# Kernel optimization log

Hardware: AMD Instinct MI355X
Metric: run time of the kernel (lower is better)

## Reference

```python
import jax, jax.numpy as jnp
import numpy as np
import math

NEG_INF = -1e9  # keras Softmax masking uses a large negative additive constant

def setup_inputs() -> dict:
    key = jax.random.key(0)
    k1, k2, k3, k4 = jax.random.split(key, 4)
    B, T, C, H = 4, 4096, 1024, 128
    x = jax.random.normal(k1, (B, T, C), dtype=jnp.float32)
    Wq = jax.random.normal(k2, (C, H), dtype=jnp.float32) * (1.0 / math.sqrt(C))
    Wk = jax.random.normal(k3, (C, H), dtype=jnp.float32) * (1.0 / math.sqrt(C))
    Wv = jax.random.normal(k4, (C, H), dtype=jnp.float32) * (1.0 / math.sqrt(C))
    return {"x": x, "Wq": Wq, "Wk": Wk, "Wv": Wv}

def reference(x, Wq, Wk, Wv):
    # x: [B, T, C]; projections are bias-free Dense layers
    B, T, C = x.shape
    q = jnp.einsum('btc,ch->bth', x, Wq)  # [B, T, H]
    k = jnp.einsum('btc,ch->bth', x, Wk)  # [B, T, H]
    v = jnp.einsum('btc,ch->bth', x, Wv)  # [B, T, H]
    # NOTE: original scales by sqrt(C) (the input channel dim), not sqrt(head_size)
    wei = jnp.einsum('bth,bsh->bts', q, k) / math.sqrt(C)  # [B, T, T]
    causal = jnp.tril(jnp.ones((T, T), dtype=bool))
    wei = jnp.where(causal[None, :, :], wei, NEG_INF)
    wei = jax.nn.softmax(wei, axis=-1)
    # dropout is identity at inference
    out = jnp.einsum('bts,bsh->bth', wei, v)  # [B, T, H]
    return out
```

## Files before the change

kernel.cpp:

```cpp
#include <hip/hip_runtime.h>
#include <hip/hip_bf16.h>

typedef __bf16 bf16x8 __attribute__((ext_vector_type(8)));
typedef __bf16 bf16x4 __attribute__((ext_vector_type(4)));
typedef float  f32x4  __attribute__((ext_vector_type(4)));

#define NB 4
#define TT 4096
#define CC 1024
#define HH 128
#define PS 72
#define MNEG -30000.0f
#define NHV 31

__device__ inline void gload16(const void* g, void* l) {
  __builtin_amdgcn_global_load_lds(
      (const __attribute__((address_space(1))) void*)g,
      (__attribute__((address_space(3))) void*)l, 16, 0, 0);
}

__device__ __forceinline__ int probe_isbf(const unsigned int* __restrict__ xw) {
  int lane = threadIdx.x & 63;
  int cnt = 0;
#pragma unroll
  for (int i = 0; i < 4; ++i) {
    unsigned int w = xw[lane + 64 * i];
    int e = (int)((w >> 7) & 0xFFu);
    cnt += (e >= 100 && e <= 135) ? 1 : 0;
  }
  cnt += __shfl_xor(cnt, 1);  cnt += __shfl_xor(cnt, 2);  cnt += __shfl_xor(cnt, 4);
  cnt += __shfl_xor(cnt, 8);  cnt += __shfl_xor(cnt, 16); cnt += __shfl_xor(cnt, 32);
  return cnt >= 128;
}

__global__ __launch_bounds__(256) void transpose_w3(
    const void* __restrict__ Wq, const void* __restrict__ Wk,
    const void* __restrict__ Wv, __bf16* __restrict__ Wt,
    const unsigned int* __restrict__ xw) {
  int isbf = probe_isbf(xw);
  int which = blockIdx.y;
  const void* W = (which == 0) ? Wq : (which == 1) ? Wk : Wv;
  int idx = blockIdx.x * 256 + threadIdx.x;
  int h = idx & 127, c = idx >> 7;
  __bf16 val;
  if (isbf) val = ((const __bf16*)W)[c * HH + h];
  else      val = (__bf16)(((const float*)W)[c * HH + h]);
  size_t o = (size_t)(c >> 6) * 24576 + (size_t)which * 8192 +
             (size_t)((c >> 3) & 7) * 1024 + (size_t)h * 8 + (c & 7);
  Wt[o] = val;
}

__global__ __launch_bounds__(768) void qkv_proj(
    const void* __restrict__ x, const __bf16* __restrict__ Wt,
    __bf16* __restrict__ q, __bf16* __restrict__ ktl, __bf16* __restrict__ vtl) {
  __shared__ __align__(16) __bf16 XT[2][4096];
  __shared__ __align__(16) __bf16 WTs[2][24576];
  int isbf = probe_isbf((const unsigned int*)x);
  int tid = threadIdx.x, lane = tid & 63, wave = tid >> 6;
  int which = wave >> 2, rowgrp = wave & 3;
  int l16 = lane & 15, quad = lane >> 4;
  int row0 = blockIdx.x * 64;
  f32x4 acc[8] = {};

#define STAGE(ss, b)                                                          \
  for (int i = wave; i < 56; i += 12) {                                       \
    if (i < 8) {                                                              \
      int row = i * 8 + (lane >> 3), g = lane & 7;                            \
      bf16x8 pk;                                                              \
      if (isbf) {                                                             \
        pk = *(const bf16x8*)((const __bf16*)x + (size_t)(row0 + row) * CC +  \
                              (ss) * 64 + g * 8);                             \
      } else {                                                                \
        const float* xf = (const float*)x + (size_t)(row0 + row) * CC +       \
                          (ss) * 64 + g * 8;                                  \
        f32x4 lo = *(const f32x4*)xf;                                         \
        f32x4 hi = *(const f32x4*)(xf + 4);                                   \
        for (int j = 0; j < 4; ++j) { pk[j] = (__bf16)lo[j]; pk[j+4] = (__bf16)hi[j]; } \
      }                                                                       \
      *(bf16x8*)(&XT[b][g * 512 + (row ^ g) * 8]) = pk;                       \
    } else {                                                                  \
      int j = i - 8;                                                          \
      gload16(Wt + (size_t)(ss) * 24576 + j * 512 + lane * 8,                 \
              &WTs[b][j * 512]);                                              \
    }                                                                         \
  }

  STAGE(0, 0);
  for (int s = 0; s < 16; ++s) {
    int cb = s & 1;
    __syncthreads();
    if (s + 1 < 16) { STAGE(s + 1, cb ^ 1); }
#pragma unroll
    for (int t = 0; t < 2; ++t) {
      int g = t * 4 + quad;
      bf16x8 a = *(const bf16x8*)(&XT[cb][g * 512 + ((rowgrp * 16 + l16) ^ g) * 8]);
#pragma unroll
      for (int nt = 0; nt < 8; ++nt) {
        bf16x8 b = *(const bf16x8*)(&WTs[cb][(size_t)which * 8192 + g * 1024 + (nt * 16 + l16) * 8]);
        acc[nt] = __builtin_amdgcn_mfma_f32_16x16x32_bf16(a, b, acc[nt], 0, 0, 0);
      }
    }
  }
#undef STAGE

  int tile = row0 >> 6;
  if (which == 0) {
#pragma unroll
    for (int nt = 0; nt < 8; ++nt)
#pragma unroll
      for (int r = 0; r < 4; ++r) {
        int row = row0 + rowgrp * 16 + quad * 4 + r;
        q[(size_t)row * HH + nt * 16 + l16] = (__bf16)acc[nt][r];
      }
  } else if (which == 1) {
    __bf16* kb = ktl + (size_t)tile * 8192;
#pragma unroll
    for (int nt = 0; nt < 8; ++nt) {
      int h = nt * 16 + l16, g = h >> 3, j = h & 7;
#pragma unroll
      for (int r = 0; r < 4; ++r) {
        int sidx = rowgrp * 16 + quad * 4 + r;
        kb[g * 512 + sidx * 8 + j] = (__bf16)acc[nt][r];
      }
    }
  } else {
    __bf16* vb = vtl + (size_t)tile * 8192;
#pragma unroll
    for (int nt = 0; nt < 8; ++nt) {
      int h = nt * 16 + l16;
      int sb = rowgrp * 16 + quad * 4;
      bf16x4 pk;
#pragma unroll
      for (int r = 0; r < 4; ++r) pk[r] = (__bf16)acc[nt][r];
      *(bf16x4*)(vb + (sb >> 3) * 1024 + h * 8 + (sb & 7)) = pk;
    }
  }
}

__global__ __launch_bounds__(768, 3) void flash_attn_bal(
    const __bf16* __restrict__ q, const __bf16* __restrict__ ktl,
    const __bf16* __restrict__ vtl, void* __restrict__ out,
    const unsigned int* __restrict__ xw,
    float* __restrict__ partO, float* __restrict__ partL) {
  __shared__ __align__(16) __bf16 PL[12][16 * PS];
  __shared__ float CMB[2][64][132];
  __shared__ float CL[2][64];

  int bx = blockIdx.x;
  int batch = (bx & 7) >> 1;
  int qt0 = ((bx >> 3) << 1) | (bx & 1);

  int tid = threadIdx.x, lane = tid & 63, wave = tid >> 6;
  int kg = wave >> 2, rowgrp = wave & 3;
  int l16 = lane & 15, quad = lane >> 4;

  int isbf = probe_isbf(xw);
  const __bf16* qp  = q   + (size_t)batch * TT * HH;
  const __bf16* ktb = ktl + (size_t)batch * TT * HH;
  const __bf16* vtb = vtl + (size_t)batch * TT * HH;

  bf16x8 onesf;
#pragma unroll
  for (int j = 0; j < 8; ++j) onesf[j] = (l16 == 0) ? (__bf16)1.0f : (__bf16)0.0f;
  const float SC = 0.0450842200278f;
  const float M0 = 4.0f;

  for (int part = 0; part < 2; ++part) {
    int qtu, j0, j1;
    if (part == 0) { qtu = qt0; j0 = 0; j1 = min(qt0 + 1, 33); }
    else {
      if (qt0 > 30) break;
      qtu = 63 - qt0; j0 = 33; j1 = 64 - qt0;
    }
    int qb = qtu * 64;
    int qrl = qb + rowgrp * 16 + quad * 4;

    bf16x8 qf[4];
    {
      const __bf16* qrow = qp + (size_t)(qb + rowgrp * 16 + l16) * HH + quad * 8;
#pragma unroll
      for (int ks = 0; ks < 4; ++ks) qf[ks] = *(const bf16x8*)(qrow + ks * 32);
    }

    f32x4 acc[8] = {};
    f32x4 acc_l = {};

    for (int jt = j0 + kg; jt < j1; jt += 3) {
      const __bf16* kt  = ktb + (size_t)jt * 8192;
      const __bf16* vt2 = vtb + (size_t)jt * 8192;

      bf16x8 kf[4][4];
#pragma unroll
      for (int ks = 0; ks < 4; ++ks)
#pragma unroll
        for (int kn = 0; kn < 4; ++kn)
          kf[ks][kn] = *(const bf16x8*)(kt + ((4 * ks + quad) * 64 + kn * 16 + l16) * 8);

      f32x4 accs[4] = {};
#pragma unroll
      for (int ks = 0; ks < 4; ++ks)
#pragma unroll
        for (int kn = 0; kn < 4; ++kn)
          accs[kn] = __builtin_amdgcn_mfma_f32_16x16x32_bf16(qf[ks], kf[ks][kn], accs[kn], 0, 0, 0);

      bf16x8 vf[2][8];
#pragma unroll
      for (int ks2 = 0; ks2 < 2; ++ks2)
#pragma unroll
        for (int nt = 0; nt < 8; ++nt)
          vf[ks2][nt] = *(const bf16x8*)(vt2 + (ks2 * 4 + quad) * 1024 + (nt * 16 + l16) * 8);

      float pv[4][4];
      if (jt == qtu) {
#pragma unroll
        for (int nt = 0; nt < 4; ++nt) {
          int kcol = jt * 64 + nt * 16 + l16;
#pragma unroll
          for (int r = 0; r < 4; ++r) {
            float z = fmaf(accs[nt][r], SC, -M0);
            z = (kcol <= qrl + r) ? z : MNEG;
            pv[nt][r] = exp2f(z);
          }
        }
      } else {
#pragma unroll
        for (int nt = 0; nt < 4; ++nt)
#pragma unroll
          for (int r = 0; r < 4; ++r)
            pv[nt][r] = exp2f(fmaf(accs[nt][r], SC, -M0));
      }

      __bf16* pw = &PL[wave][0];
#pragma unroll
      for (int nt = 0; nt < 4; ++nt)
#pragma unroll
        for (int r = 0; r < 4; ++r)
          pw[(quad * 4 + r) * PS + nt * 16 + l16] = (__bf16)pv[nt][r];

#pragma unroll
      for (int ks2 = 0; ks2 < 2; ++ks2) {
        bf16x8 pa = *(const bf16x8*)(pw + l16 * PS + ks2 * 32 + quad * 8);
        acc_l = __builtin_amdgcn_mfma_f32_16x16x32_bf16(pa, onesf, acc_l, 0, 0, 0);
#pragma unroll
        for (int nt = 0; nt < 8; ++nt)
          acc[nt] = __builtin_amdgcn_mfma_f32_16x16x32_bf16(pa, vf[ks2][nt], acc[nt], 0, 0, 0);
      }
    }

    int rr = rowgrp * 16 + quad * 4;
    __syncthreads();
    if (kg > 0) {
#pragma unroll
      for (int nt = 0; nt < 8; ++nt)
#pragma unroll
        for (int r = 0; r < 4; ++r)
          CMB[kg - 1][rr + r][nt * 16 + l16] = acc[nt][r];
      if (l16 == 0) {
#pragma unroll
        for (int r = 0; r < 4; ++r) CL[kg - 1][rr + r] = acc_l[r];
      }
    }
    __syncthreads();
    if (kg == 0) {
      float lsum[4];
#pragma unroll
      for (int r = 0; r < 4; ++r) {
        float lr = __shfl(acc_l[r], lane & 48);
        lsum[r] = lr + CL[0][rr + r] + CL[1][rr + r];
      }
      if (part == 0 && qt0 <= 32) {
        __bf16* ob = (__bf16*)out + (size_t)batch * TT * HH;
        float*  of = (float*)out  + (size_t)batch * TT * HH;
        float inv[4];
#pragma unroll
        for (int r = 0; r < 4; ++r) inv[r] = 1.f / fmaxf(lsum[r], 1e-30f);
#pragma unroll
        for (int nt = 0; nt < 8; ++nt)
#pragma unroll
          for (int r = 0; r < 4; ++r) {
            int col = nt * 16 + l16;
            float val = (acc[nt][r] + CMB[0][rr + r][col] + CMB[1][rr + r][col]) * inv[r];
            size_t idx = (size_t)(qb + rr + r) * HH + col;
            if (isbf) ob[idx] = (__bf16)val;
            else      of[idx] = val;
          }
      } else {
        int slot = (batch * NHV + (qtu - 33)) * 2 + part;
        float* po = partO + (size_t)slot * 8192;
#pragma unroll
        for (int nt = 0; nt < 8; ++nt)
#pragma unroll
          for (int r = 0; r < 4; ++r) {
            int col = nt * 16 + l16;
            po[(rr + r) * 128 + col] = acc[nt][r] + CMB[0][rr + r][col] + CMB[1][rr + r][col];
          }
        if (l16 == 0) {
#pragma unroll
          for (int r = 0; r < 4; ++r) partL[slot * 64 + rr + r] = lsum[r];
        }
      }
    }
  }
}

__global__ __launch_bounds__(256) void combine2(
    const float* __restrict__ partO, const float* __restrict__ partL,
    void* __restrict__ out, const unsigned int* __restrict__ xw) {
  int bx = blockIdx.x;
  int batch = bx / NHV, qidx = bx % NHV;
  int Q = 33 + qidx;
  int slot0 = (batch * NHV + qidx) * 2;
  __shared__ float inv[64];
  int tid = threadIdx.x;
  if (tid < 64) {
    float L = partL[slot0 * 64 + tid] + partL[(slot0 + 1) * 64 + tid];
    inv[tid] = 1.f / fmaxf(L, 1e-30f);
  }
  __syncthreads();
  int isbf = probe_isbf(xw);
  size_t obase = (size_t)batch * TT * HH + (size_t)Q * 8192;
  const f32x4* p4 = (const f32x4*)partO;
#pragma unroll
  for (int i = 0; i < 8; ++i) {
    int e4 = i * 256 + tid;
    int row = e4 >> 5;
    f32x4 a = p4[(size_t)slot0 * 2048 + e4];
    f32x4 b = p4[(size_t)(slot0 + 1) * 2048 + e4];
    float w = inv[row];
    f32x4 v;
    v[0] = (a[0] + b[0]) * w; v[1] = (a[1] + b[1]) * w;
    v[2] = (a[2] + b[2]) * w; v[3] = (a[3] + b[3]) * w;
    if (isbf) {
      bf16x4 ob;
#pragma unroll
      for (int j = 0; j < 4; ++j) ob[j] = (__bf16)v[j];
      *(bf16x4*)((__bf16*)out + obase + (size_t)e4 * 4) = ob;
    } else {
      *(f32x4*)((float*)out + obase + (size_t)e4 * 4) = v;
    }
  }
}

__global__ __launch_bounds__(768, 3) void flash_attn_fb(
    const __bf16* __restrict__ q, const __bf16* __restrict__ ktl,
    const __bf16* __restrict__ vtl, void* __restrict__ out,
    const unsigned int* __restrict__ xw) {
  __shared__ __align__(16) __bf16 PLs[6][2][32 * PS];
  __shared__ float CMB[4][32][132];
  __shared__ float CL[4][32];

  int bx = blockIdx.x;
  int batch = (bx & 7) >> 1;
  int qt0 = ((bx >> 3) << 1) | (bx & 1);

  int tid = threadIdx.x, lane = tid & 63, wave = tid >> 6;
  int p = wave >> 1, rw = wave & 1;
  int l16 = lane & 15, quad = lane >> 4;

  int kA = (6 * (qt0 + 1) + 32) / 65;
  kA = max(1, min(5, kA));
  int qtB = 63 - qt0;
  int unit, kg, nkg, qtu, rbase;
  if (p < kA) { unit = 0; kg = p;      nkg = kA;     qtu = qt0; rbase = 0;  }
  else        { unit = 1; kg = p - kA; nkg = 6 - kA; qtu = qtB; rbase = 32; }

  int qb = qtu * 64;
  int MAXT = max(qt0 / kA + 1, qtB / (6 - kA) + 1);
  int mytrips = (qtu - kg) / nkg + 1;
  int isbf = probe_isbf(xw);

  const __bf16* qp  = q   + (size_t)batch * TT * HH;
  const __bf16* ktb = ktl + (size_t)batch * TT * HH;
  const __bf16* vtb = vtl + (size_t)batch * TT * HH;

  bf16x8 qf[2][4];
#pragma unroll
  for (int rg = 0; rg < 2; ++rg) {
    const __bf16* qrow = qp + (size_t)(qb + rbase + rg * 16 + l16) * HH + quad * 8;
#pragma unroll
    for (int ks = 0; ks < 4; ++ks) qf[rg][ks] = *(const bf16x8*)(qrow + ks * 32);
  }
  bf16x8 onesf;
#pragma unroll
  for (int j = 0; j < 8; ++j) onesf[j] = (l16 == 0) ? (__bf16)1.0f : (__bf16)0.0f;

  f32x4 acc_o[2][4] = {};
  f32x4 acc_l[2] = {};
  const float SC = 0.0450842200278f;
  const float M0 = 4.0f;

  for (int t = 0; t < MAXT; ++t) {
    int jt = kg + t * nkg;
    int valid = (t < mytrips);
    int jtc = valid ? jt : kg;
    const __bf16* kt  = ktb + (size_t)jtc * 8192;
    const __bf16* vt2 = vtb + (size_t)jtc * 8192;

    bf16x8 kf[4][2];
#pragma unroll
    for (int ks = 0; ks < 4; ++ks)
#pragma unroll
      for (int kn = 0; kn < 2; ++kn)
        kf[ks][kn] = *(const bf16x8*)(kt + ((4 * ks + quad) * 64 + (rw * 2 + kn) * 16 + l16) * 8);

    f32x4 accs[2][2] = {};
#pragma unroll
    for (int ks = 0; ks < 4; ++ks)
#pragma unroll
      for (int rg = 0; rg < 2; ++rg)
#pragma unroll
        for (int kn = 0; kn < 2; ++kn)
          accs[rg][kn] = __builtin_amdgcn_mfma_f32_16x16x32_bf16(qf[rg][ks], kf[ks][kn], accs[rg][kn], 0, 0, 0);

    bf16x8 vf[2][4];
#pragma unroll
    for (int ks2 = 0; ks2 < 2; ++ks2)
#pragma unroll
      for (int nt = 0; nt < 4; ++nt)
        vf[ks2][nt] = *(const bf16x8*)(vt2 + (ks2 * 4 + quad) * 1024 + (rw * 64 + nt * 16 + l16) * 8);

    float pv[2][2][4];
    if (valid && jt == qtu) {
#pragma unroll
      for (int rg = 0; rg < 2; ++rg)
#pragma unroll
        for (int kn = 0; kn < 2; ++kn) {
          int kcol = jt * 64 + (rw * 2 + kn) * 16 + l16;
          int qr0 = qb + rbase + rg * 16 + quad * 4;
#pragma unroll
          for (int r = 0; r < 4; ++r) {
            float z = fmaf(accs[rg][kn][r], SC, -M0);
            z = (kcol <= qr0 + r) ? z : MNEG;
            pv[rg][kn][r] = exp2f(z);
          }
        }
    } else if (valid) {
#pragma unroll
      for (int rg = 0; rg < 2; ++rg)
#pragma unroll
        for (int kn = 0; kn < 2; ++kn)
#pragma unroll
          for (int r = 0; r < 4; ++r)
            pv[rg][kn][r] = exp2f(fmaf(accs[rg][kn][r], SC, -M0));
    } else {
#pragma unroll
      for (int rg = 0; rg < 2; ++rg)
#pragma unroll
        for (int kn = 0; kn < 2; ++kn)
#pragma unroll
          for (int r = 0; r < 4; ++r)
            pv[rg][kn][r] = 0.0f;
    }

    __bf16* pw = &PLs[p][t & 1][0];
#pragma unroll
    for (int rg = 0; rg < 2; ++rg)
#pragma unroll
      for (int kn = 0; kn < 2; ++kn)
#pragma unroll
        for (int r = 0; r < 4; ++r)
          pw[(rg * 16 + quad * 4 + r) * PS + (rw * 2 + kn) * 16 + l16] = (__bf16)pv[rg][kn][r];

    __syncthreads();

#pragma unroll
    for (int ks2 = 0; ks2 < 2; ++ks2) {
      bf16x8 pa0 = *(const bf16x8*)(pw + l16 * PS + ks2 * 32 + quad * 8);
      bf16x8 pa1 = *(const bf16x8*)(pw + (16 + l16) * PS + ks2 * 32 + quad * 8);
      acc_l[0] = __builtin_amdgcn_mfma_f32_16x16x32_bf16(pa0, onesf, acc_l[0], 0, 0, 0);
      acc_l[1] = __builtin_amdgcn_mfma_f32_16x16x32_bf16(pa1, onesf, acc_l[1], 0, 0, 0);
#pragma unroll
      for (int nt = 0; nt < 4; ++nt) {
        acc_o[0][nt] = __builtin_amdgcn_mfma_f32_16x16x32_bf16(pa0, vf[ks2][nt], acc_o[0][nt], 0, 0, 0);
        acc_o[1][nt] = __builtin_amdgcn_mfma_f32_16x16x32_bf16(pa1, vf[ks2][nt], acc_o[1][nt], 0, 0, 0);
      }
    }
  }

  if (kg > 0) {
    int slot = (unit == 0) ? (kg - 1) : (kA - 1 + kg - 1);
#pragma unroll
    for (int rh = 0; rh < 2; ++rh)
#pragma unroll
      for (int nt = 0; nt < 4; ++nt)
#pragma unroll
        for (int r = 0; r < 4; ++r)
          CMB[slot][rh * 16 + quad * 4 + r][rw * 64 + nt * 16 + l16] = acc_o[rh][nt][r];
    if (rw == 0 && l16 == 0) {
#pragma unroll
      for (int rh = 0; rh < 2; ++rh)
#pragma unroll
        for (int r = 0; r < 4; ++r) CL[slot][rh * 16 + quad * 4 + r] = acc_l[rh][r];
    }
  }
  __syncthreads();
  if (kg == 0) {
    int lo  = (unit == 0) ? 0 : kA - 1;
    int cnt = (unit == 0) ? kA - 1 : 5 - kA;
    __bf16* ob = (__bf16*)out + (size_t)batch * TT * HH;
    float*  of = (float*)out  + (size_t)batch * TT * HH;
#pragma unroll
    for (int rh = 0; rh < 2; ++rh) {
      float inv[4];
#pragma unroll
      for (int r = 0; r < 4; ++r) {
        float lr = __shfl(acc_l[rh][r], lane & 48);
        for (int c = 0; c < cnt; ++c) lr += CL[lo + c][rh * 16 + quad * 4 + r];
        inv[r] = 1.f / fmaxf(lr, 1e-30f);
      }
#pragma unroll
      for (int nt = 0; nt < 4; ++nt)
#pragma unroll
        for (int r = 0; r < 4; ++r) {
          int row = qb + rbase + rh * 16 + quad * 4 + r;
          int col = rw * 64 + nt * 16 + l16;
          float val = acc_o[rh][nt][r];
          for (int c = 0; c < cnt; ++c) val += CMB[lo + c][rh * 16 + quad * 4 + r][col];
          val *= inv[r];
          size_t idx = (size_t)row * HH + col;
          if (isbf) ob[idx] = (__bf16)val;
          else      of[idx] = val;
        }
    }
  }
}

extern "C" void kernel_launch(void* const* d_in, const int* in_sizes, int n_in,
                              void* d_out, int out_size, void* d_ws, size_t ws_size,
                              hipStream_t stream) {
  const void* x  = d_in[0];
  const void* Wq = d_in[1];
  const void* Wk = d_in[2];
  const void* Wv = d_in[3];
  char* wsb = (char*)d_ws;
  __bf16* q   = (__bf16*)wsb;
  __bf16* ktl = q   + (size_t)NB * TT * HH;
  __bf16* vtl = ktl + (size_t)NB * TT * HH;
  __bf16* wt  = vtl + (size_t)NB * TT * HH;
  size_t base = (((size_t)(3 * NB * TT * HH + 3 * CC * HH) * 2) + 255) & ~(size_t)255;
  size_t needO = (size_t)NB * NHV * 2 * 8192 * 4;
  size_t needL = (size_t)NB * NHV * 2 * 64 * 4;
  float* partO = (float*)(wsb + base);
  float* partL = (float*)(wsb + base + needO);
  bool bal = (base + needO + needL) <= ws_size;
  (void)in_sizes; (void)n_in; (void)out_size;

  transpose_w3<<<dim3(512, 3), 256, 0, stream>>>(Wq, Wk, Wv, wt,
                                                 (const unsigned int*)x);
  qkv_proj<<<256, 768, 0, stream>>>(x, wt, q, ktl, vtl);
  if (bal) {
    flash_attn_bal<<<NB * 64, 768, 0, stream>>>(q, ktl, vtl, d_out,
                                                (const unsigned int*)x,
                                                partO, partL);
    combine2<<<NB * NHV, 256, 0, stream>>>(partO, partL, d_out,
                                           (const unsigned int*)x);
  } else {
    flash_attn_fb<<<NB * 64, 768, 0, stream>>>(q, ktl, vtl, d_out,
                                               (const unsigned int*)x);
  }
}
```

Measured before the change: 173.9 us.

## Fuse split-KV combine into attention kernel via inter-block flag handoff

Removes the separate combine2 kernel launch. Now only the part-1 block writes its partial O and L to the workspace and raises a per-tile flag. The part-0 block spins on that flag and then merges the partial into its own accumulator and writes the final output. This saves one launch and half the partial-buffer traffic. In exchange it adds spin-waiting that can deadlock if the producer block is not resident at the same time as the waiting block.

```diff
diff --git a/kernel.cpp b/kernel.cpp
--- a/kernel.cpp
+++ b/kernel.cpp
@@ -36,7 +36,9 @@
 __global__ __launch_bounds__(256) void transpose_w3(
     const void* __restrict__ Wq, const void* __restrict__ Wk,
     const void* __restrict__ Wv, __bf16* __restrict__ Wt,
-    const unsigned int* __restrict__ xw) {
+    const unsigned int* __restrict__ xw, unsigned int* __restrict__ flags) {
+  if (blockIdx.x == 0 && blockIdx.y == 0 && threadIdx.x < NB * NHV)
+    flags[threadIdx.x] = 0u;
   int isbf = probe_isbf(xw);
   int which = blockIdx.y;
   const void* W = (which == 0) ? Wq : (which == 1) ? Wk : Wv;
@@ -141,7 +143,8 @@
     const __bf16* __restrict__ q, const __bf16* __restrict__ ktl,
     const __bf16* __restrict__ vtl, void* __restrict__ out,
     const unsigned int* __restrict__ xw,
-    float* __restrict__ partO, float* __restrict__ partL) {
+    float* __restrict__ partO, float* __restrict__ partL,
+    unsigned int* __restrict__ flags) {
   __shared__ __align__(16) __bf16 PL[12][16 * PS];
   __shared__ float CMB[2][64][132];
   __shared__ float CL[2][64];
@@ -284,8 +287,8 @@
             if (isbf) ob[idx] = (__bf16)val;
             else      of[idx] = val;
           }
-      } else {
-        int slot = (batch * NHV + (qtu - 33)) * 2 + part;
+      } else if (part == 1) {
+        int slot = batch * NHV + (qtu - 33);
         float* po = partO + (size_t)slot * 8192;
 #pragma unroll
         for (int nt = 0; nt < 8; ++nt)
@@ -298,45 +301,40 @@
 #pragma unroll
           for (int r = 0; r < 4; ++r) partL[slot * 64 + rr + r] = lsum[r];
         }
-      }
-    }
-  }
-}
-
-__global__ __launch_bounds__(256) void combine2(
-    const float* __restrict__ partO, const float* __restrict__ partL,
-    void* __restrict__ out, const unsigned int* __restrict__ xw) {
-  int bx = blockIdx.x;
-  int batch = bx / NHV, qidx = bx % NHV;
-  int Q = 33 + qidx;
-  int slot0 = (batch * NHV + qidx) * 2;
-  __shared__ float inv[64];
-  int tid = threadIdx.x;
-  if (tid < 64) {
-    float L = partL[slot0 * 64 + tid] + partL[(slot0 + 1) * 64 + tid];
-    inv[tid] = 1.f / fmaxf(L, 1e-30f);
-  }
-  __syncthreads();
-  int isbf = probe_isbf(xw);
-  size_t obase = (size_t)batch * TT * HH + (size_t)Q * 8192;
-  const f32x4* p4 = (const f32x4*)partO;
-#pragma unroll
-  for (int i = 0; i < 8; ++i) {
-    int e4 = i * 256 + tid;
-    int row = e4 >> 5;
-    f32x4 a = p4[(size_t)slot0 * 2048 + e4];
-    f32x4 b = p4[(size_t)(slot0 + 1) * 2048 + e4];
-    float w = inv[row];
-    f32x4 v;
-    v[0] = (a[0] + b[0]) * w; v[1] = (a[1] + b[1]) * w;
-    v[2] = (a[2] + b[2]) * w; v[3] = (a[3] + b[3]) * w;
-    if (isbf) {
-      bf16x4 ob;
-#pragma unroll
-      for (int j = 0; j < 4; ++j) ob[j] = (__bf16)v[j];
-      *(bf16x4*)((__bf16*)out + obase + (size_t)e4 * 4) = ob;
-    } else {
-      *(f32x4*)((float*)out + obase + (size_t)e4 * 4) = v;
+      } else {
+        int slot = batch * NHV + (qt0 - 33);
+        unsigned int done = 0;
+        while (!done) {
+          if (lane == 0) done = atomicAdd(&flags[slot], 0u);
+          done = __shfl(done, 0);
+        }
+        __threadfence();
+        const float* po = partO + (size_t)slot * 8192;
+        float inv[4];
+#pragma unroll
+        for (int r = 0; r < 4; ++r) {
+          float L = lsum[r] + partL[slot * 64 + rr + r];
+          inv[r] = 1.f / fmaxf(L, 1e-30f);
+        }
+        __bf16* ob = (__bf16*)out + (size_t)batch * TT * HH;
+        float*  of = (float*)out  + (size_t)batch * TT * HH;
+#pragma unroll
+        for (int nt = 0; nt < 8; ++nt)
+#pragma unroll
+          for (int r = 0; r < 4; ++r) {
+            int col = nt * 16 + l16;
+            float val = (acc[nt][r] + CMB[0][rr + r][col] + CMB[1][rr + r][col] +
+                         po[(rr + r) * 128 + col]) * inv[r];
+            size_t idx = (size_t)(qb + rr + r) * HH + col;
+            if (isbf) ob[idx] = (__bf16)val;
+            else      of[idx] = val;
+          }
+      }
+    }
+    if (part == 1) {
+      __threadfence();
+      __syncthreads();
+      if (tid == 0) atomicExch(&flags[batch * NHV + (qtu - 33)], 1u);
     }
   }
 }
@@ -538,22 +536,22 @@
   __bf16* vtl = ktl + (size_t)NB * TT * HH;
   __bf16* wt  = vtl + (size_t)NB * TT * HH;
   size_t base = (((size_t)(3 * NB * TT * HH + 3 * CC * HH) * 2) + 255) & ~(size_t)255;
-  size_t needO = (size_t)NB * NHV * 2 * 8192 * 4;
-  size_t needL = (size_t)NB * NHV * 2 * 64 * 4;
+  size_t needO = (size_t)NB * NHV * 8192 * 4;
+  size_t needL = (size_t)NB * NHV * 64 * 4;
+  size_t needF = (size_t)NB * NHV * 4;
   float* partO = (float*)(wsb + base);
   float* partL = (float*)(wsb + base + needO);
-  bool bal = (base + needO + needL) <= ws_size;
+  unsigned int* flags = (unsigned int*)(wsb + base + needO + needL);
+  bool bal = (base + needO + needL + needF) <= ws_size;
   (void)in_sizes; (void)n_in; (void)out_size;
 
   transpose_w3<<<dim3(512, 3), 256, 0, stream>>>(Wq, Wk, Wv, wt,
-                                                 (const unsigned int*)x);
+                                                 (const unsigned int*)x, flags);
   qkv_proj<<<256, 768, 0, stream>>>(x, wt, q, ktl, vtl);
   if (bal) {
     flash_attn_bal<<<NB * 64, 768, 0, stream>>>(q, ktl, vtl, d_out,
                                                 (const unsigned int*)x,
-                                                partO, partL);
-    combine2<<<NB * NHV, 256, 0, stream>>>(partO, partL, d_out,
-                                           (const unsigned int*)x);
+                                                partO, partL, flags);
   } else {
     flash_attn_fb<<<NB * 64, 768, 0, stream>>>(q, ktl, vtl, d_out,
                                                (const unsigned int*)x);
```

Measured after the change: 224.2 us. 1.29x slower.
